# Performance work log

Hardware: AMD Instinct MI355X
Metric: run time of the kernel (lower is better)

The kernel has to match this reference:

```python
import math
import jax, jax.numpy as jnp
import numpy as np

BS, N, NH_N, NH_E, NH_Y, H = 2, 256, 256, 128, 128, 8
F = NH_N // H  # per-head feature dim


def _lin(x, w, b):
    # w stored as (in, out): out = x @ w + b
    return x @ w + b


def setup_inputs() -> dict:
    key = jax.random.key(0)
    ks = iter(jax.random.split(key, 64))
    def w(shape, s=0.02):
        return jax.random.normal(next(ks), shape, dtype=jnp.float32) * s
    inp = {
        'x': jax.random.normal(next(ks), (BS, N, NH_N), dtype=jnp.float32),
        'a': jax.random.normal(next(ks), (BS, N, N, NH_E), dtype=jnp.float32),
        'y': jax.random.normal(next(ks), (BS, NH_Y), dtype=jnp.float32),
        'qw': w((NH_N, NH_N)), 'qb': w((NH_N,)),
        'kw': w((NH_N, NH_N)), 'kb': w((NH_N,)),
        'vw': w((NH_N, NH_N)), 'vb': w((NH_N,)),
        'a2x_add_w': w((NH_E, NH_N)), 'a2x_add_b': w((NH_N,)),
        'a2x_mul_w': w((NH_E, NH_N)), 'a2x_mul_b': w((NH_N,)),
        'y2e_mul_w': w((NH_Y, NH_N)), 'y2e_mul_b': w((NH_N,)),
        'y2e_add_w': w((NH_Y, NH_N)), 'y2e_add_b': w((NH_N,)),
        'y2x_mul_w': w((NH_Y, NH_N)), 'y2x_mul_b': w((NH_N,)),
        'y2x_add_w': w((NH_Y, NH_N)), 'y2x_add_b': w((NH_N,)),
        'y_y_w': w((NH_Y, NH_Y)), 'y_y_b': w((NH_Y,)),
        'x_y_w': w((4 * NH_N, NH_Y)), 'x_y_b': w((NH_Y,)),
        'a_y_w': w((4 * NH_E, NH_Y)), 'a_y_b': w((NH_Y,)),
        'x_out_w': w((NH_N, NH_N)), 'x_out_b': w((NH_N,)),
        'a_out_w': w((NH_N, NH_E)), 'a_out_b': w((NH_E,)),
        'y_out1_w': w((NH_Y, NH_Y)), 'y_out1_b': w((NH_Y,)),
        'y_out2_w': w((NH_Y, NH_Y)), 'y_out2_b': w((NH_Y,)),
    }
    return inp


def reference(x, a, y, qw, qb, kw, kb, vw, vb,
              a2x_add_w, a2x_add_b, a2x_mul_w, a2x_mul_b,
              y2e_mul_w, y2e_mul_b, y2e_add_w, y2e_add_b,
              y2x_mul_w, y2x_mul_b, y2x_add_w, y2x_add_b,
              y_y_w, y_y_b, x_y_w, x_y_b, a_y_w, a_y_b,
              x_out_w, x_out_b, a_out_w, a_out_b,
              y_out1_w, y_out1_b, y_out2_w, y_out2_b):
    bs, n, _ = x.shape
    Q = _lin(x, qw, qb).reshape(bs, n, H, F)
    K = _lin(x, kw, kb).reshape(bs, n, H, F)
    # Feature-wise outer product (never reduced over F): (bs, n, n, H, F)
    Y = (Q[:, :, None] * K[:, None, :]) / math.sqrt(F)
    a1 = _lin(a, a2x_add_w, a2x_add_b).reshape(bs, n, n, H, F)
    a2 = _lin(a, a2x_mul_w, a2x_mul_b).reshape(bs, n, n, H, F)
    Y = Y * (a1 + 1.0) + a2
    # edge output path
    ahat = Y.reshape(bs, n, n, NH_N)
    ye1 = _lin(y, y2e_add_w, y2e_add_b)[:, None, None]
    ye2 = _lin(y, y2e_mul_w, y2e_mul_b)[:, None, None]
    ahat = _lin(ye1 + (ye2 + 1.0) * ahat, a_out_w, a_out_b)
    # node output path: softmax over the second node axis (dim=2)
    attn = jax.nn.softmax(Y, axis=2)
    V = _lin(x, vw, vb).reshape(bs, n, H, F)
    wV = jnp.einsum('bijhf,bjhf->bihf', attn, V).reshape(bs, n, NH_N)
    yx1 = _lin(y, y2x_add_w, y2x_add_b)[:, None]
    yx2 = _lin(y, y2x_mul_w, y2x_mul_b)[:, None]
    xhat = _lin(yx1 + (yx2 + 1.0) * wV, x_out_w, x_out_b)
    # global output path (Xtoy / Atoy use unbiased std, ddof=1 as in torch.std)
    zx = jnp.concatenate([x.mean(axis=1), x.min(axis=1), x.max(axis=1),
                          jnp.std(x, axis=1, ddof=1)], axis=-1)
    za = jnp.concatenate([a.mean(axis=(1, 2)), a.min(axis=(1, 2)), a.max(axis=(1, 2)),
                          jnp.std(a, axis=(1, 2), ddof=1)], axis=-1)
    yhat = _lin(y, y_y_w, y_y_b) + _lin(za, a_y_w, a_y_b) + _lin(zx, x_y_w, x_y_b)
    yhat = _lin(jax.nn.relu(_lin(yhat, y_out1_w, y_out1_b)), y_out2_w, y_out2_b)
    return (xhat, ahat, yhat)
```

## Files before the change

kernel.cpp:

```cpp
#include <hip/hip_runtime.h>
#include <hip/hip_bf16.h>
#include <cstddef>

constexpr int BS = 2;
constexpr int N  = 256;
constexpr int D  = 256;
constexpr int E  = 128;
constexpr int YD = 128;
constexpr float RSQRT_F = 0.17677669529663687f;

typedef __attribute__((ext_vector_type(8))) short     short8;
typedef __attribute__((ext_vector_type(4))) float     f32x4;
typedef __attribute__((ext_vector_type(4))) unsigned short u16x4;
typedef __attribute__((ext_vector_type(8))) unsigned short u16x8;

__device__ __forceinline__ unsigned short f2bf(float x) {
    unsigned u = __float_as_uint(x);
    unsigned r = (u + 0x7fffu + ((u >> 16) & 1u)) >> 16;
    return (unsigned short)r;
}
__device__ __forceinline__ float bf2f(unsigned short h) {
    return __uint_as_float(((unsigned)h) << 16);
}
__device__ __forceinline__ f32x4 mfma16(short8 a, short8 b, f32x4 c) {
    return __builtin_amdgcn_mfma_f32_16x16x32_bf16(a, b, c, 0, 0, 0);
}

__global__ __launch_bounds__(256) void prep_kernel(
        const float* __restrict__ x, const float* __restrict__ a,
        const float* __restrict__ y,
        const float* __restrict__ qw, const float* __restrict__ qb,
        const float* __restrict__ kw, const float* __restrict__ kb,
        const float* __restrict__ vw, const float* __restrict__ vb,
        const float* __restrict__ Wadd, const float* __restrict__ Wmul,
        const float* __restrict__ W2,
        const float* __restrict__ we_add, const float* __restrict__ be_add,
        const float* __restrict__ we_mul, const float* __restrict__ be_mul,
        const float* __restrict__ wx_add, const float* __restrict__ bx_add,
        const float* __restrict__ wx_mul, const float* __restrict__ bx_mul,
        float* __restrict__ Q, unsigned short* __restrict__ kvJ,
        unsigned short* __restrict__ WaddT, unsigned short* __restrict__ WmulT,
        unsigned short* __restrict__ W2T,
        float* __restrict__ ye1, float* __restrict__ ye2,
        float* __restrict__ yx1, float* __restrict__ yx2,
        float* __restrict__ psum, float* __restrict__ psumsq,
        float* __restrict__ pmin, float* __restrict__ pmax,
        float* __restrict__ zx) {
    const int blk = blockIdx.x;
    const int tid = threadIdx.x;
    __shared__ float smem[4096];

    if (blk < 192) {
        const int m  = blk >> 6;
        const int rg = blk & 63;
        const float* W = (m == 0) ? qw : (m == 1) ? kw : vw;
        const float* B = (m == 0) ? qb : (m == 1) ? kb : vb;
        float (*xs)[D] = (float(*)[D])smem;
#pragma unroll
        for (int r = 0; r < 8; ++r)
            xs[r][tid] = x[(size_t)(rg * 8 + r) * D + tid];
        __syncthreads();
        float acc[8];
        const float bb = B[tid];
#pragma unroll
        for (int r = 0; r < 8; ++r) acc[r] = bb;
#pragma unroll 4
        for (int k = 0; k < D; ++k) {
            const float w = W[k * D + tid];
#pragma unroll
            for (int r = 0; r < 8; ++r) acc[r] += xs[r][k] * w;
        }
#pragma unroll
        for (int r = 0; r < 8; ++r) {
            const int row = rg * 8 + r;
            if (m == 0) Q[(size_t)row * D + tid] = acc[r];
            else        kvJ[((size_t)row * D + tid) * 2 + (m - 1)] = f2bf(acc[r]);
        }
    } else if (blk < 576) {
        int idx = (blk - 192) * 256 + tid;
        int s = idx >> 15;
        int k = idx & 32767;
        if (s == 0)      { int f = k >> 7, e = k & 127; WaddT[k] = f2bf(Wadd[e * 256 + f]); }
        else if (s == 1) { int f = k >> 7, e = k & 127; WmulT[k] = f2bf(Wmul[e * 256 + f]); }
        else             { int f = k & 255, e = k >> 8; W2T[k]   = f2bf(W2[f * 128 + e]); }
    } else if (blk < 584) {
        const int bb = (blk - 576) >> 2;
        const int m  = (blk - 576) & 3;
        const float* W; const float* B; float* O;
        switch (m) {
            case 0:  W = we_add; B = be_add; O = ye1; break;
            case 1:  W = we_mul; B = be_mul; O = ye2; break;
            case 2:  W = wx_add; B = bx_add; O = yx1; break;
            default: W = wx_mul; B = bx_mul; O = yx2; break;
        }
        float acc = B[tid];
#pragma unroll 4
        for (int k = 0; k < YD; ++k)
            acc += y[bb * YD + k] * W[k * D + tid];
        O[bb * D + tid] = acc;
    } else if (blk < 600) {
        const int bb = (blk - 584) >> 3;
        const int fc = (blk - 584) & 7;
        const int fl = tid & 31;
        const int ig = tid >> 5;
        const int f  = fc * 32 + fl;
        float s = 0.f, ss = 0.f, mn = INFINITY, mx = -INFINITY;
#pragma unroll 4
        for (int i = ig * 32; i < ig * 32 + 32; ++i) {
            const float v = x[((size_t)bb * N + i) * D + f];
            s += v; ss += v * v; mn = fminf(mn, v); mx = fmaxf(mx, v);
        }
        smem[0 * 256 + ig * 32 + fl] = s;
        smem[1 * 256 + ig * 32 + fl] = ss;
        smem[2 * 256 + ig * 32 + fl] = mn;
        smem[3 * 256 + ig * 32 + fl] = mx;
        __syncthreads();
        if (ig == 0) {
#pragma unroll
            for (int gg = 1; gg < 8; ++gg) {
                s += smem[0 * 256 + gg * 32 + fl]; ss += smem[1 * 256 + gg * 32 + fl];
                mn = fminf(mn, smem[2 * 256 + gg * 32 + fl]);
                mx = fmaxf(mx, smem[3 * 256 + gg * 32 + fl]);
            }
            const float M = 256.f;
            const float mean = s / M;
            const float var  = (ss - s * s / M) / (M - 1.f);
            zx[bb * 1024 + f]       = mean;
            zx[bb * 1024 + 256 + f] = mn;
            zx[bb * 1024 + 512 + f] = mx;
            zx[bb * 1024 + 768 + f] = sqrtf(fmaxf(var, 0.f));
        }
    } else {
        const int bi2 = blk - 600;
        const int te  = tid & 31;
        const int tj  = tid >> 5;
        const float* base = a + (size_t)bi2 * N * E + te * 4;
        f32x4 s4  = (f32x4){0.f, 0.f, 0.f, 0.f};
        f32x4 ss4 = (f32x4){0.f, 0.f, 0.f, 0.f};
        f32x4 mn4 = (f32x4){INFINITY, INFINITY, INFINITY, INFINITY};
        f32x4 mx4 = (f32x4){-INFINITY, -INFINITY, -INFINITY, -INFINITY};
#pragma unroll 8
        for (int j = tj * 32; j < tj * 32 + 32; ++j) {
            const f32x4 v = *(const f32x4*)(base + (size_t)j * E);
            s4 += v;
            ss4.x = fmaf(v.x, v.x, ss4.x); ss4.y = fmaf(v.y, v.y, ss4.y);
            ss4.z = fmaf(v.z, v.z, ss4.z); ss4.w = fmaf(v.w, v.w, ss4.w);
            mn4.x = fminf(mn4.x, v.x); mn4.y = fminf(mn4.y, v.y);
            mn4.z = fminf(mn4.z, v.z); mn4.w = fminf(mn4.w, v.w);
            mx4.x = fmaxf(mx4.x, v.x); mx4.y = fmaxf(mx4.y, v.y);
            mx4.z = fmaxf(mx4.z, v.z); mx4.w = fmaxf(mx4.w, v.w);
        }
        *(f32x4*)(smem + (0 * 8 + tj) * 128 + te * 4) = s4;
        *(f32x4*)(smem + (1 * 8 + tj) * 128 + te * 4) = ss4;
        *(f32x4*)(smem + (2 * 8 + tj) * 128 + te * 4) = mn4;
        *(f32x4*)(smem + (3 * 8 + tj) * 128 + te * 4) = mx4;
        __syncthreads();
        if (tid < 128) {
            float s = 0.f, ss = 0.f, mn = INFINITY, mx = -INFINITY;
#pragma unroll
            for (int g = 0; g < 8; ++g) {
                s  += smem[(0 * 8 + g) * 128 + tid];
                ss += smem[(1 * 8 + g) * 128 + tid];
                mn = fminf(mn, smem[(2 * 8 + g) * 128 + tid]);
                mx = fmaxf(mx, smem[(3 * 8 + g) * 128 + tid]);
            }
            const int o = bi2 * E + tid;
            psum[o] = s; psumsq[o] = ss; pmin[o] = mn; pmax[o] = mx;
        }
    }
}

__global__ __launch_bounds__(512, 1) void main_kernel(
        const float* __restrict__ a,
        const unsigned short* __restrict__ WaddT, const float* __restrict__ Badd,
        const unsigned short* __restrict__ WmulT, const float* __restrict__ Bmul,
        const unsigned short* __restrict__ W2T,  const float* __restrict__ AoutB,
        const float* __restrict__ Q, const unsigned short* __restrict__ kvJ,
        const float* __restrict__ ye1, const float* __restrict__ ye2,
        float* __restrict__ ahat, float* __restrict__ wV) {
    const int bi = ((blockIdx.x & 7) << 6) | (blockIdx.x >> 3);
    const int b  = bi >> 8;
    const int tid  = threadIdx.x;
    const int lane = tid & 63;
    const int w    = tid >> 6;
    const int l15  = lane & 15;
    const int lk   = lane >> 4;

    __shared__ unsigned short abuf[2][32 * 128];
    __shared__ unsigned short hbuf[2][32 * 256];

    const float* arow = a + (size_t)bi * (N * E);
    float* ahatp      = ahat + (size_t)bi * (N * E);
    const unsigned short* kvb = kvJ + (size_t)b * N * D * 2;

    short8 waf[4][2], wmf[4][2], w2f[8];
#pragma unroll
    for (int ks = 0; ks < 4; ++ks)
#pragma unroll
        for (int m_ = 0; m_ < 2; ++m_) {
            const int frow = w * 32 + m_ * 16 + l15;
            waf[ks][m_] = *(const short8*)(WaddT + frow * 128 + ks * 32 + lk * 8);
            wmf[ks][m_] = *(const short8*)(WmulT + frow * 128 + ks * 32 + lk * 8);
        }
#pragma unroll
    for (int ks = 0; ks < 8; ++ks)
        w2f[ks] = *(const short8*)(W2T + (w * 16 + l15) * 256 + ks * 32 + lk * 8);

    float qs[8], e1c[8], e2c[8], b1c[8], b2c[8];
#pragma unroll
    for (int m_ = 0; m_ < 2; ++m_) {
        const int f0 = w * 32 + m_ * 16 + lk * 4;
        const f32x4 qv = *(const f32x4*)(Q + (size_t)bi * D + f0);
        const f32x4 a1 = *(const f32x4*)(ye1 + b * D + f0);
        const f32x4 a2 = *(const f32x4*)(ye2 + b * D + f0);
        const f32x4 bb1 = *(const f32x4*)(Badd + f0);
        const f32x4 bb2 = *(const f32x4*)(Bmul + f0);
#pragma unroll
        for (int r = 0; r < 4; ++r) {
            const int fi = m_ * 4 + r;
            qs[fi]  = qv[r] * RSQRT_F;
            e1c[fi] = a1[r];
            e2c[fi] = a2[r] + 1.f;
            b1c[fi] = bb1[r] + 1.f;
            b2c[fi] = bb2[r];
        }
    }
    const f32x4 bias2 = *(const f32x4*)(AoutB + w * 16 + lk * 4);

    float sm_l[8], sm_a[8];
#pragma unroll
    for (int q = 0; q < 8; ++q) { sm_l[q] = 0.f; sm_a[q] = 0.f; }

    const int sjl = tid >> 4;
    const int seq = tid & 15;
    const unsigned saddr = ((unsigned)(sjl * 256 + seq * 16)) ^ ((unsigned)(sjl & 7) << 4);

    {
        const float* ap = arow + (size_t)sjl * E + seq * 8;
        const f32x4 v0 = *(const f32x4*)ap;
        const f32x4 v1 = *(const f32x4*)(ap + 4);
        u16x8 pk;
        pk.s0 = f2bf(v0.x); pk.s1 = f2bf(v0.y); pk.s2 = f2bf(v0.z); pk.s3 = f2bf(v0.w);
        pk.s4 = f2bf(v1.x); pk.s5 = f2bf(v1.y); pk.s6 = f2bf(v1.z); pk.s7 = f2bf(v1.w);
        *(u16x8*)((char*)abuf[0] + saddr) = pk;
    }
    __syncthreads();

    for (int t = 0; t < 8; ++t) {
        const int j0 = t * 32;
        const unsigned short* ab = abuf[t & 1];
        unsigned short* hw = hbuf[t & 1];

        f32x4 p0, p1;
        if (t < 7) {
            const float* ap = arow + (size_t)(j0 + 32 + sjl) * E + seq * 8;
            p0 = *(const f32x4*)ap;
            p1 = *(const f32x4*)(ap + 4);
        }
        u16x8 kvv[2][2];
#pragma unroll
        for (int n_ = 0; n_ < 2; ++n_) {
            const int jg = j0 + n_ * 16 + l15;
#pragma unroll
            for (int m_ = 0; m_ < 2; ++m_)
                kvv[n_][m_] = *(const u16x8*)(kvb + ((size_t)jg * D + w * 32 + m_ * 16 + lk * 4) * 2);
        }

        f32x4 acc1[2][2], acc2[2][2];
#pragma unroll
        for (int m_ = 0; m_ < 2; ++m_) {
            const f32x4 i1 = (f32x4){b1c[m_ * 4 + 0], b1c[m_ * 4 + 1], b1c[m_ * 4 + 2], b1c[m_ * 4 + 3]};
            const f32x4 i2 = (f32x4){b2c[m_ * 4 + 0], b2c[m_ * 4 + 1], b2c[m_ * 4 + 2], b2c[m_ * 4 + 3]};
#pragma unroll
            for (int n_ = 0; n_ < 2; ++n_) { acc1[m_][n_] = i1; acc2[m_][n_] = i2; }
        }
#pragma unroll
        for (int ks = 0; ks < 4; ++ks) {
            short8 bfrg[2];
#pragma unroll
            for (int n_ = 0; n_ < 2; ++n_) {
                const int jrow = n_ * 16 + l15;
                const unsigned baddr = ((unsigned)(jrow * 256 + (ks * 32 + lk * 8) * 2))
                                       ^ ((unsigned)(jrow & 7) << 4);
                bfrg[n_] = *(const short8*)((const char*)ab + baddr);
            }
#pragma unroll
            for (int m_ = 0; m_ < 2; ++m_)
#pragma unroll
                for (int n_ = 0; n_ < 2; ++n_) {
                    acc1[m_][n_] = mfma16(waf[ks][m_], bfrg[n_], acc1[m_][n_]);
                    acc2[m_][n_] = mfma16(wmf[ks][m_], bfrg[n_], acc2[m_][n_]);
                }
        }

#pragma unroll
        for (int n_ = 0; n_ < 2; ++n_) {
            const int jrow = n_ * 16 + l15;
#pragma unroll
            for (int m_ = 0; m_ < 2; ++m_) {
                u16x4 hp;
#pragma unroll
                for (int r = 0; r < 4; ++r) {
                    const int fi = m_ * 4 + r;
                    const float kf = bf2f(kvv[n_][m_][2 * r]);
                    const float vf = bf2f(kvv[n_][m_][2 * r + 1]);
                    const float yv = qs[fi] * kf * acc1[m_][n_][r] + acc2[m_][n_][r];
                    hp[r] = f2bf(e1c[fi] + e2c[fi] * yv);
                    const float ev = __expf(yv);
                    sm_l[fi] += ev;
                    sm_a[fi] += ev * vf;
                }
                const unsigned haddr = ((unsigned)(jrow * 512 + (w * 32 + m_ * 16 + lk * 4) * 2))
                                       ^ ((unsigned)(jrow & 7) << 4);
                *(u16x4*)((char*)hw + haddr) = hp;
            }
        }

        if (t < 7) {
            u16x8 pk;
            pk.s0 = f2bf(p0.x); pk.s1 = f2bf(p0.y); pk.s2 = f2bf(p0.z); pk.s3 = f2bf(p0.w);
            pk.s4 = f2bf(p1.x); pk.s5 = f2bf(p1.y); pk.s6 = f2bf(p1.z); pk.s7 = f2bf(p1.w);
            *(u16x8*)((char*)abuf[(t + 1) & 1] + saddr) = pk;
        }
        __syncthreads();

        f32x4 accO[2];
        accO[0] = bias2; accO[1] = bias2;
#pragma unroll
        for (int ks = 0; ks < 8; ++ks) {
            const int foff = ks * 32 + lk * 8;
#pragma unroll
            for (int n2 = 0; n2 < 2; ++n2) {
                const int jrow = n2 * 16 + l15;
                const unsigned haddr = ((unsigned)(jrow * 512 + foff * 2))
                                       ^ ((unsigned)(jrow & 7) << 4);
                const short8 hf = *(const short8*)((const char*)hw + haddr);
                accO[n2] = mfma16(w2f[ks], hf, accO[n2]);
            }
        }
        {
            const int eb = w * 16 + lk * 4;
#pragma unroll
            for (int n2 = 0; n2 < 2; ++n2) {
                const int jg2 = j0 + n2 * 16 + l15;
                *(f32x4*)(ahatp + (size_t)jg2 * E + eb) = accO[n2];
            }
        }
    }

#pragma unroll
    for (int st = 1; st <= 8; st <<= 1) {
#pragma unroll
        for (int fi = 0; fi < 8; ++fi) {
            sm_l[fi] += __shfl_xor(sm_l[fi], st, 64);
            sm_a[fi] += __shfl_xor(sm_a[fi], st, 64);
        }
    }
    if (l15 == 0) {
#pragma unroll
        for (int m_ = 0; m_ < 2; ++m_)
#pragma unroll
            for (int r = 0; r < 4; ++r) {
                const int fi = m_ * 4 + r;
                const int f  = w * 32 + m_ * 16 + lk * 4 + r;
                wV[(size_t)bi * D + f] = sm_a[fi] / sm_l[fi];
            }
    }
}

__global__ __launch_bounds__(256) void post_kernel(
        const float* __restrict__ wV,
        const float* __restrict__ yx1, const float* __restrict__ yx2,
        const float* __restrict__ W, const float* __restrict__ B,
        const float* __restrict__ psum, const float* __restrict__ psumsq,
        const float* __restrict__ pmin, const float* __restrict__ pmax,
        float* __restrict__ xhat, float* __restrict__ za) {
    const int blk = blockIdx.x;
    const int tid = threadIdx.x;
    __shared__ float smem[2048];

    if (blk < 64) {
        float (*xr)[D] = (float(*)[D])smem;
#pragma unroll
        for (int r = 0; r < 8; ++r) {
            const int row = blk * 8 + r;
            const int b = row >> 8;
            xr[r][tid] = yx1[b * D + tid] + (yx2[b * D + tid] + 1.f) * wV[(size_t)row * D + tid];
        }
        __syncthreads();
        float acc[8];
        const float bb = B[tid];
#pragma unroll
        for (int r = 0; r < 8; ++r) acc[r] = bb;
#pragma unroll 4
        for (int k = 0; k < D; ++k) {
            const float w = W[k * D + tid];
#pragma unroll
            for (int r = 0; r < 8; ++r) acc[r] += xr[r][k] * w;
        }
#pragma unroll
        for (int r = 0; r < 8; ++r)
            xhat[(size_t)(blk * 8 + r) * D + tid] = acc[r];
    } else {
        const int b = blk - 64;
        const int feat = tid & 127;
        const int g = tid >> 7;
        float s = 0.f, ss = 0.f, mn = INFINITY, mx = -INFINITY;
#pragma unroll 4
        for (int c = g * 128; c < g * 128 + 128; ++c) {
            const int o = (b * 256 + c) * E + feat;
            s += psum[o]; ss += psumsq[o];
            mn = fminf(mn, pmin[o]); mx = fmaxf(mx, pmax[o]);
        }
        smem[0 * 256 + g * 128 + feat] = s;
        smem[1 * 256 + g * 128 + feat] = ss;
        smem[2 * 256 + g * 128 + feat] = mn;
        smem[3 * 256 + g * 128 + feat] = mx;
        __syncthreads();
        if (g == 0) {
            s += smem[0 * 256 + 128 + feat]; ss += smem[1 * 256 + 128 + feat];
            mn = fminf(mn, smem[2 * 256 + 128 + feat]);
            mx = fmaxf(mx, smem[3 * 256 + 128 + feat]);
            const float M = 65536.f;
            const float mean = s / M;
            const float var  = (ss - s * s / M) / (M - 1.f);
            za[b * 512 + feat]       = mean;
            za[b * 512 + 128 + feat] = mn;
            za[b * 512 + 256 + feat] = mx;
            za[b * 512 + 384 + feat] = sqrtf(fmaxf(var, 0.f));
        }
    }
}

__global__ __launch_bounds__(128) void yhat_partial_kernel(
        const float* __restrict__ y,
        const float* __restrict__ za, const float* __restrict__ zx,
        const float* __restrict__ yyw, const float* __restrict__ ayw,
        const float* __restrict__ xyw,
        float* __restrict__ partial) {
    const int bb = blockIdx.x / 52;
    const int c  = blockIdx.x - bb * 52;
    const int o  = threadIdx.x;
    const int k0 = c * 32;
    float p = 0.f;
    if (k0 < 128) {
#pragma unroll 8
        for (int k = k0; k < k0 + 32; ++k) p += y[bb * YD + k] * yyw[k * YD + o];
    } else if (k0 < 640) {
        const int kk = k0 - 128;
#pragma unroll 8
        for (int k = kk; k < kk + 32; ++k) p += za[bb * 512 + k] * ayw[k * YD + o];
    } else {
        const int kk = k0 - 640;
#pragma unroll 8
        for (int k = kk; k < kk + 32; ++k) p += zx[bb * 1024 + k] * xyw[k * YD + o];
    }
    partial[(bb * 52 + c) * YD + o] = p;
}

__global__ __launch_bounds__(512) void yhat_finish_kernel(
        const float* __restrict__ partial,
        const float* __restrict__ yyb, const float* __restrict__ xyb,
        const float* __restrict__ ayb,
        const float* __restrict__ w1, const float* __restrict__ b1,
        const float* __restrict__ w2, const float* __restrict__ b2,
        float* __restrict__ out) {
    const int b = blockIdx.x;
    const int tid = threadIdx.x;
    const int o = tid & 127;
    const int q = tid >> 7;
    __shared__ float red[4][128];
    __shared__ float h1s[128], h2s[128];
    float s = 0.f;
#pragma unroll 13
    for (int c = q * 13; c < q * 13 + 13; ++c)
        s += partial[(b * 52 + c) * YD + o];
    red[q][o] = s;
    __syncthreads();
    if (tid < 128)
        h1s[o] = yyb[o] + xyb[o] + ayb[o] + red[0][o] + red[1][o] + red[2][o] + red[3][o];
    __syncthreads();
    float p2 = 0.f;
#pragma unroll 8
    for (int k = q * 32; k < q * 32 + 32; ++k) p2 += h1s[k] * w1[k * YD + o];
    red[q][o] = p2;
    __syncthreads();
    if (tid < 128) h2s[o] = fmaxf(b1[o] + red[0][o] + red[1][o] + red[2][o] + red[3][o], 0.f);
    __syncthreads();
    float p3 = 0.f;
#pragma unroll 8
    for (int k = q * 32; k < q * 32 + 32; ++k) p3 += h2s[k] * w2[k * YD + o];
    red[q][o] = p3;
    __syncthreads();
    if (tid < 128) out[b * YD + o] = b2[o] + red[0][o] + red[1][o] + red[2][o] + red[3][o];
}

extern "C" void kernel_launch(void* const* d_in, const int* in_sizes, int n_in,
                              void* d_out, int out_size, void* d_ws, size_t ws_size,
                              hipStream_t stream) {
    const float* x         = (const float*)d_in[0];
    const float* a         = (const float*)d_in[1];
    const float* y         = (const float*)d_in[2];
    const float* qw        = (const float*)d_in[3];  const float* qb        = (const float*)d_in[4];
    const float* kw        = (const float*)d_in[5];  const float* kb        = (const float*)d_in[6];
    const float* vw        = (const float*)d_in[7];  const float* vb        = (const float*)d_in[8];
    const float* a2x_add_w = (const float*)d_in[9];  const float* a2x_add_b = (const float*)d_in[10];
    const float* a2x_mul_w = (const float*)d_in[11]; const float* a2x_mul_b = (const float*)d_in[12];
    const float* y2e_mul_w = (const float*)d_in[13]; const float* y2e_mul_b = (const float*)d_in[14];
    const float* y2e_add_w = (const float*)d_in[15]; const float* y2e_add_b = (const float*)d_in[16];
    const float* y2x_mul_w = (const float*)d_in[17]; const float* y2x_mul_b = (const float*)d_in[18];
    const float* y2x_add_w = (const float*)d_in[19]; const float* y2x_add_b = (const float*)d_in[20];
    const float* y_y_w     = (const float*)d_in[21]; const float* y_y_b     = (const float*)d_in[22];
    const float* x_y_w     = (const float*)d_in[23]; const float* x_y_b     = (const float*)d_in[24];
    const float* a_y_w     = (const float*)d_in[25]; const float* a_y_b     = (const float*)d_in[26];
    const float* x_out_w   = (const float*)d_in[27]; const float* x_out_b   = (const float*)d_in[28];
    const float* a_out_w   = (const float*)d_in[29]; const float* a_out_b   = (const float*)d_in[30];
    const float* y_out1_w  = (const float*)d_in[31]; const float* y_out1_b  = (const float*)d_in[32];
    const float* y_out2_w  = (const float*)d_in[33]; const float* y_out2_b  = (const float*)d_in[34];

    float* ws = (float*)d_ws;
    float* Q      = ws;
    unsigned short* kvJ = (unsigned short*)(ws + 131072);
    float* wV     = ws + 262144;
    float* ye1    = ws + 393216;
    float* ye2    = ws + 393728;
    float* yx1    = ws + 394240;
    float* yx2    = ws + 394752;
    float* psum   = ws + 395264;
    float* psumsq = ws + 460800;
    float* pminb  = ws + 526336;
    float* pmaxb  = ws + 591872;
    float* za     = ws + 657408;
    float* zx     = ws + 658432;
    unsigned short* WaddT = (unsigned short*)(ws + 660480);
    unsigned short* WmulT = (unsigned short*)(ws + 676864);
    unsigned short* W2T   = (unsigned short*)(ws + 693248);
    float* ypart  = ws + 709632;

    float* xhat = (float*)d_out;
    float* ahat = (float*)d_out + 131072;
    float* yhat = (float*)d_out + 16908288;

    prep_kernel<<<1112, 256, 0, stream>>>(
        x, a, y, qw, qb, kw, kb, vw, vb,
        a2x_add_w, a2x_mul_w, a_out_w,
        y2e_add_w, y2e_add_b, y2e_mul_w, y2e_mul_b,
        y2x_add_w, y2x_add_b, y2x_mul_w, y2x_mul_b,
        Q, kvJ, WaddT, WmulT, W2T,
        ye1, ye2, yx1, yx2,
        psum, psumsq, pminb, pmaxb, zx);
    main_kernel<<<512, 512, 0, stream>>>(a, WaddT, a2x_add_b, WmulT, a2x_mul_b,
                                         W2T, a_out_b, Q, kvJ, ye1, ye2, ahat, wV);
    post_kernel<<<66, 256, 0, stream>>>(wV, yx1, yx2, x_out_w, x_out_b,
                                        psum, psumsq, pminb, pmaxb, xhat, za);
    yhat_partial_kernel<<<104, 128, 0, stream>>>(y, za, zx, y_y_w, a_y_w, x_y_w, ypart);
    yhat_finish_kernel<<<2, 512, 0, stream>>>(ypart, y_y_b, x_y_b, a_y_b,
                                              y_out1_w, y_out1_b, y_out2_w, y_out2_b, yhat);
}
```

Baseline: 116.1 us.

## Move edge-tensor statistics reduction from prep kernel into main kernel's odd blocks

The per-row reduction of the edge tensor (sum, sum of squares, min, max) moves out of the prep kernel and into the main kernel. Odd blocks of a doubled main grid compute these statistics using 512 threads and the shared hbuf scratch, while even blocks do the original edge/attention work. The goal is to overlap the bandwidth-heavy statistics pass with the compute-bound main work, shrink the prep kernel, and perhaps let the second read of the edge tensor hit in cache. In exchange the main kernel launches twice as many blocks under launch_bounds(512,1), so the statistics blocks may compete for CUs with the main-work blocks.

```diff
diff --git a/kernel.cpp b/kernel.cpp
--- a/kernel.cpp
+++ b/kernel.cpp
@@ -27,7 +27,7 @@
 }
 
 __global__ __launch_bounds__(256) void prep_kernel(
-        const float* __restrict__ x, const float* __restrict__ a,
+        const float* __restrict__ x,
         const float* __restrict__ y,
         const float* __restrict__ qw, const float* __restrict__ qb,
         const float* __restrict__ kw, const float* __restrict__ kb,
@@ -43,12 +43,10 @@
         unsigned short* __restrict__ W2T,
         float* __restrict__ ye1, float* __restrict__ ye2,
         float* __restrict__ yx1, float* __restrict__ yx2,
-        float* __restrict__ psum, float* __restrict__ psumsq,
-        float* __restrict__ pmin, float* __restrict__ pmax,
         float* __restrict__ zx) {
     const int blk = blockIdx.x;
     const int tid = threadIdx.x;
-    __shared__ float smem[4096];
+    __shared__ float smem[2048];
 
     if (blk < 192) {
         const int m  = blk >> 6;
@@ -98,7 +96,7 @@
         for (int k = 0; k < YD; ++k)
             acc += y[bb * YD + k] * W[k * D + tid];
         O[bb * D + tid] = acc;
-    } else if (blk < 600) {
+    } else {
         const int bb = (blk - 584) >> 3;
         const int fc = (blk - 584) & 7;
         const int fl = tid & 31;
@@ -130,8 +128,26 @@
             zx[bb * 1024 + 512 + f] = mx;
             zx[bb * 1024 + 768 + f] = sqrtf(fmaxf(var, 0.f));
         }
-    } else {
-        const int bi2 = blk - 600;
+    }
+}
+
+__global__ __launch_bounds__(512, 1) void main_kernel(
+        const float* __restrict__ a,
+        const unsigned short* __restrict__ WaddT, const float* __restrict__ Badd,
+        const unsigned short* __restrict__ WmulT, const float* __restrict__ Bmul,
+        const unsigned short* __restrict__ W2T,  const float* __restrict__ AoutB,
+        const float* __restrict__ Q, const unsigned short* __restrict__ kvJ,
+        const float* __restrict__ ye1, const float* __restrict__ ye2,
+        float* __restrict__ ahat, float* __restrict__ wV,
+        float* __restrict__ psum, float* __restrict__ psumsq,
+        float* __restrict__ pmin, float* __restrict__ pmax) {
+    const int tid  = threadIdx.x;
+
+    __shared__ unsigned short abuf[2][32 * 128];
+    __shared__ unsigned short hbuf[2][32 * 256];
+
+    if (blockIdx.x & 1) {
+        const int bi2 = blockIdx.x >> 1;
         const int te  = tid & 31;
         const int tj  = tid >> 5;
         const float* base = a + (size_t)bi2 * N * E + te * 4;
@@ -140,7 +156,7 @@
         f32x4 mn4 = (f32x4){INFINITY, INFINITY, INFINITY, INFINITY};
         f32x4 mx4 = (f32x4){-INFINITY, -INFINITY, -INFINITY, -INFINITY};
 #pragma unroll 8
-        for (int j = tj * 32; j < tj * 32 + 32; ++j) {
+        for (int j = tj * 16; j < tj * 16 + 16; ++j) {
             const f32x4 v = *(const f32x4*)(base + (size_t)j * E);
             s4 += v;
             ss4.x = fmaf(v.x, v.x, ss4.x); ss4.y = fmaf(v.y, v.y, ss4.y);
@@ -150,44 +166,34 @@
             mx4.x = fmaxf(mx4.x, v.x); mx4.y = fmaxf(mx4.y, v.y);
             mx4.z = fmaxf(mx4.z, v.z); mx4.w = fmaxf(mx4.w, v.w);
         }
-        *(f32x4*)(smem + (0 * 8 + tj) * 128 + te * 4) = s4;
-        *(f32x4*)(smem + (1 * 8 + tj) * 128 + te * 4) = ss4;
-        *(f32x4*)(smem + (2 * 8 + tj) * 128 + te * 4) = mn4;
-        *(f32x4*)(smem + (3 * 8 + tj) * 128 + te * 4) = mx4;
+        float* sc = (float*)hbuf;
+        *(f32x4*)(sc + (0 * 16 + tj) * 128 + te * 4) = s4;
+        *(f32x4*)(sc + (1 * 16 + tj) * 128 + te * 4) = ss4;
+        *(f32x4*)(sc + (2 * 16 + tj) * 128 + te * 4) = mn4;
+        *(f32x4*)(sc + (3 * 16 + tj) * 128 + te * 4) = mx4;
         __syncthreads();
         if (tid < 128) {
             float s = 0.f, ss = 0.f, mn = INFINITY, mx = -INFINITY;
 #pragma unroll
-            for (int g = 0; g < 8; ++g) {
-                s  += smem[(0 * 8 + g) * 128 + tid];
-                ss += smem[(1 * 8 + g) * 128 + tid];
-                mn = fminf(mn, smem[(2 * 8 + g) * 128 + tid]);
-                mx = fmaxf(mx, smem[(3 * 8 + g) * 128 + tid]);
+            for (int g = 0; g < 16; ++g) {
+                s  += sc[(0 * 16 + g) * 128 + tid];
+                ss += sc[(1 * 16 + g) * 128 + tid];
+                mn = fminf(mn, sc[(2 * 16 + g) * 128 + tid]);
+                mx = fmaxf(mx, sc[(3 * 16 + g) * 128 + tid]);
             }
             const int o = bi2 * E + tid;
             psum[o] = s; psumsq[o] = ss; pmin[o] = mn; pmax[o] = mx;
         }
-    }
-}
-
-__global__ __launch_bounds__(512, 1) void main_kernel(
-        const float* __restrict__ a,
-        const unsigned short* __restrict__ WaddT, const float* __restrict__ Badd,
-        const unsigned short* __restrict__ WmulT, const float* __restrict__ Bmul,
-        const unsigned short* __restrict__ W2T,  const float* __restrict__ AoutB,
-        const float* __restrict__ Q, const unsigned short* __restrict__ kvJ,
-        const float* __restrict__ ye1, const float* __restrict__ ye2,
-        float* __restrict__ ahat, float* __restrict__ wV) {
-    const int bi = ((blockIdx.x & 7) << 6) | (blockIdx.x >> 3);
+        return;
+    }
+
+    const int k512 = blockIdx.x >> 1;
+    const int bi = ((k512 & 7) << 6) | (k512 >> 3);
     const int b  = bi >> 8;
-    const int tid  = threadIdx.x;
     const int lane = tid & 63;
     const int w    = tid >> 6;
     const int l15  = lane & 15;
     const int lk   = lane >> 4;
-
-    __shared__ unsigned short abuf[2][32 * 128];
-    __shared__ unsigned short hbuf[2][32 * 256];
 
     const float* arow = a + (size_t)bi * (N * E);
     float* ahatp      = ahat + (size_t)bi * (N * E);
@@ -541,16 +547,16 @@
     float* ahat = (float*)d_out + 131072;
     float* yhat = (float*)d_out + 16908288;
 
-    prep_kernel<<<1112, 256, 0, stream>>>(
-        x, a, y, qw, qb, kw, kb, vw, vb,
+    prep_kernel<<<600, 256, 0, stream>>>(
+        x, y, qw, qb, kw, kb, vw, vb,
         a2x_add_w, a2x_mul_w, a_out_w,
         y2e_add_w, y2e_add_b, y2e_mul_w, y2e_mul_b,
         y2x_add_w, y2x_add_b, y2x_mul_w, y2x_mul_b,
         Q, kvJ, WaddT, WmulT, W2T,
-        ye1, ye2, yx1, yx2,
-        psum, psumsq, pminb, pmaxb, zx);
-    main_kernel<<<512, 512, 0, stream>>>(a, WaddT, a2x_add_b, WmulT, a2x_mul_b,
-                                         W2T, a_out_b, Q, kvJ, ye1, ye2, ahat, wV);
+        ye1, ye2, yx1, yx2, zx);
+    main_kernel<<<1024, 512, 0, stream>>>(a, WaddT, a2x_add_b, WmulT, a2x_mul_b,
+                                          W2T, a_out_b, Q, kvJ, ye1, ye2, ahat, wV,
+                                          psum, psumsq, pminb, pmaxb);
     post_kernel<<<66, 256, 0, stream>>>(wV, yx1, yx2, x_out_w, x_out_b,
                                         psum, psumsq, pminb, pmaxb, xhat, za);
     yhat_partial_kernel<<<104, 128, 0, stream>>>(y, za, zx, y_y_w, a_y_w, x_y_w, ypart);
```

Result: slower. 166.5 us (+43.4%).
